# Kernel optimization log

Measured on AMD Instinct MI355X. Metric: run time of the kernel, lower is better.

## Reference

```python
import jax, jax.numpy as jnp
import numpy as np
import math

NUM_GRIDS = 128
INPUT_DIM = 128
OUTPUT_DIM = 128
BATCH = 8192
INIT_SCALE = 0.1


def _borders_cdf_grid(n_chunks):
    # inverse Laplace CDF grid borders, exactly as in the torch module
    def inv(u):
        return np.log(2.0 * u) if u <= 0.5 else -np.log(2.0 * (1.0 - u))
    cs = 1.0 / n_chunks
    b = [inv(i * cs) for i in range(1, n_chunks)]
    left = b[0] - (b[1] - b[0])
    right = b[-1] + (b[-1] - b[-2])
    return np.array([left] + b + [right], dtype=np.float32)  # [n_chunks+1]


def setup_inputs() -> dict:
    key = jax.random.key(0)
    kx, kp = jax.random.split(key)
    x = jax.random.normal(kx, (INPUT_DIM, BATCH), dtype=jnp.float32)
    s = INIT_SCALE / math.sqrt(INPUT_DIM)
    func_parameter = jax.random.uniform(
        kp, (NUM_GRIDS + 1, OUTPUT_DIM, INPUT_DIM), dtype=jnp.float32,
        minval=-s, maxval=s)
    borders = jnp.asarray(_borders_cdf_grid(NUM_GRIDS))
    inverse_chunk_lengths = 1.0 / (borders[1:] - borders[:-1])  # [NUM_GRIDS]
    return {"x": x, "func_parameter": func_parameter,
            "borders": borders, "inverse_chunk_lengths": inverse_chunk_lengths}


def reference(x, func_parameter, borders, inverse_chunk_lengths):
    # x: [I, B]; func_parameter: [G+1, O, I]
    G = borders.shape[0] - 1
    I = x.shape[0]
    # Laplace CDF: R -> [0, 1]
    exp_na = jnp.exp(-jnp.abs(x))
    cdf = jnp.where(x > 0, 1.0 - 0.5 * exp_na, 0.5 * exp_na)
    # bucketize on uniform CDF grid (truncation == floor since cdf*G >= 0)
    idx = jnp.clip((cdf * G).astype(jnp.int32), 0, G - 1)        # [I, B]
    idx_next = jnp.clip(idx + 1, 0, G)                           # [I, B]
    left = borders[idx]                                          # [I, B]
    inv_len = inverse_chunk_lengths[idx]                         # [I, B]
    d = (x - left) * inv_len                                     # [I, B]
    # gather per-input-dim parameter rows: val[i, b, o] = P[idx[i,b], o, i]
    Pt = jnp.transpose(func_parameter, (2, 0, 1))                # [I, G+1, O]
    rows = jnp.arange(I)[:, None]                                # [I, 1]
    val_l = Pt[rows, idx]                                        # [I, B, O]
    val_r = Pt[rows, idx_next]                                   # [I, B, O]
    out = ((1.0 - d)[..., None] * val_l + d[..., None] * val_r).sum(axis=0)  # [B, O]
    return out.T                                                 # [O, B]
```

## Files before the change

kernel.cpp:

```cpp
#include <hip/hip_runtime.h>
#include <cstdint>


#define NG 128
#define NI 128
#define NO 128
#define NB 8192

using half2v = __attribute__((ext_vector_type(2))) _Float16;

__device__ inline uint32_t pack_f16x2(float lo, float hi) {
    _Float16 hl = (_Float16)lo, hh = (_Float16)hi;
    return (uint32_t)__builtin_bit_cast(unsigned short, hl) |
           ((uint32_t)__builtin_bit_cast(unsigned short, hh) << 16);
}

__global__ __launch_bounds__(256) void build_q(const float* __restrict__ P,
                                               uint32_t* __restrict__ Q) {
    __shared__ float lp[32][129];
    __shared__ float ln[32][129];
    const int g  = blockIdx.x >> 2;
    const int o0 = (blockIdx.x & 3) * 32;
    const int t  = threadIdx.x;
    #pragma unroll
    for (int p = 0; p < 16; ++p) {
        int e = p * 256 + t;
        int ol = e >> 7, i = e & 127;
        lp[ol][i] = P[(size_t)(g * NO + o0 + ol) * NI + i];
        ln[ol][i] = P[(size_t)((g + 1) * NO + o0 + ol) * NI + i];
    }
    __syncthreads();
    #pragma unroll
    for (int p = 0; p < 16; ++p) {
        int e = p * 256 + t;
        int i = e >> 5, ol = e & 31;
        float pl = lp[ol][i];
        float dd = ln[ol][i] - pl;
        Q[((size_t)i * NG + g) * NO + o0 + ol] = pack_f16x2(pl, dd);
    }
}

__global__ __launch_bounds__(256) void build_t(const float* __restrict__ x,
                                               const float* __restrict__ borders,
                                               const float* __restrict__ icl,
                                               uint32_t* __restrict__ T) {
    __shared__ uint32_t lt[32][33];
    const int bi = blockIdx.x & 3;
    const int bb = blockIdx.x >> 2;
    const int t  = threadIdx.x;
    #pragma unroll
    for (int p = 0; p < 4; ++p) {
        int e = p * 256 + t;
        int il = e >> 5, bl = e & 31;
        float xv = x[(size_t)(bi * 32 + il) * NB + bb * 32 + bl];
        float ea = __expf(-fabsf(xv));
        float cdf = xv > 0.f ? 1.f - 0.5f * ea : 0.5f * ea;
        int idx = (int)(cdf * 128.f);
        idx = idx > 127 ? 127 : idx;
        float d = (xv - borders[idx]) * icl[idx];
        _Float16 hd = (_Float16)d;
        lt[il][bl] = (uint32_t)idx |
                     ((uint32_t)__builtin_bit_cast(unsigned short, hd) << 16);
    }
    __syncthreads();
    #pragma unroll
    for (int p = 0; p < 4; ++p) {
        int e = p * 256 + t;
        int bl = e >> 5, il = e & 31;
        T[(size_t)(bb * 32 + bl) * NI + bi * 32 + il] = lt[il][bl];
    }
}

__global__ __launch_bounds__(256) void main_k(const uint32_t* __restrict__ Q,
                                              const uint32_t* __restrict__ T,
                                              float* __restrict__ out) {
    __shared__ float sout[4][129];
    const int t    = threadIdx.x;
    const int wv   = t >> 6;
    const int lane = t & 63;
    const int b0   = blockIdx.x * 4;
    int b = __builtin_amdgcn_readfirstlane(b0 + wv);
    const uint32_t* __restrict__ trow = T + (size_t)b * NI;
    const int o0 = lane * 2;
    float acc0 = 0.f, acc1 = 0.f;
    #pragma unroll 8
    for (int i = 0; i < NI; ++i) {
        uint32_t tw  = trow[i];
        uint32_t idx = tw & 0xFFFFu;
        uint32_t wb  = (tw & 0xFFFF0000u) | 0x3C00u;
        const uint32_t* qrow = Q + ((size_t)((i << 7) + (int)idx) << 7);
        uint32_t q0 = qrow[o0];
        uint32_t q1 = qrow[o0 + 1];
        half2v w2 = __builtin_bit_cast(half2v, wb);
        acc0 = __builtin_amdgcn_fdot2(__builtin_bit_cast(half2v, q0), w2, acc0, false);
        acc1 = __builtin_amdgcn_fdot2(__builtin_bit_cast(half2v, q1), w2, acc1, false);
    }
    sout[wv][o0]     = acc0;
    sout[wv][o0 + 1] = acc1;
    __syncthreads();
    #pragma unroll
    for (int p = 0; p < 2; ++p) {
        int e = p * 256 + t;
        int bl = e & 3, o = e >> 2;
        out[(size_t)o * NB + b0 + bl] = sout[bl][o];
    }
}

extern "C" void kernel_launch(void* const* d_in, const int* in_sizes, int n_in,
                              void* d_out, int out_size, void* d_ws, size_t ws_size,
                              hipStream_t stream) {
    const float* x       = (const float*)d_in[0];
    const float* P       = (const float*)d_in[1];
    const float* borders = (const float*)d_in[2];
    const float* icl     = (const float*)d_in[3];
    float* out = (float*)d_out;

    uint32_t* Q = (uint32_t*)d_ws;
    uint32_t* T = Q + (size_t)NI * NG * NO;

    hipLaunchKernelGGL(build_q, dim3(NG * 4), dim3(256), 0, stream, P, Q);
    hipLaunchKernelGGL(build_t, dim3((NB / 32) * 4), dim3(256), 0, stream,
                       x, borders, icl, T);
    hipLaunchKernelGGL(main_k, dim3(NB / 4), dim3(256), 0, stream, Q, T, out);
}
```

Baseline: 111.7 us.

## Keep T in input-major layout and split main kernel over output slices

build_t now writes T in x's natural [I,B] layout with vectorized float4 loads and uint4 stores, dropping the shared-memory transpose. main_k is restructured so each block covers 32 batch columns and a 16-wide output slice: 8 lanes share one batch element and each lane loads a uint2 of Q. The output tile is then written coalesced along the batch dimension with nontemporal stores. This is meant to give better output coalescing and locality in the Q gather, at the cost of more gather instructions per useful output and a T read strided by NB.

```diff
diff --git a/kernel.cpp b/kernel.cpp
--- a/kernel.cpp
+++ b/kernel.cpp
@@ -44,65 +44,62 @@
                                                const float* __restrict__ borders,
                                                const float* __restrict__ icl,
                                                uint32_t* __restrict__ T) {
-    __shared__ uint32_t lt[32][33];
-    const int bi = blockIdx.x & 3;
-    const int bb = blockIdx.x >> 2;
-    const int t  = threadIdx.x;
+    const int e0 = (blockIdx.x * 256 + threadIdx.x) * 4;
+    const float4 xv = *(const float4*)(x + e0);
+    uint32_t r[4];
+    const float xs[4] = {xv.x, xv.y, xv.z, xv.w};
     #pragma unroll
-    for (int p = 0; p < 4; ++p) {
-        int e = p * 256 + t;
-        int il = e >> 5, bl = e & 31;
-        float xv = x[(size_t)(bi * 32 + il) * NB + bb * 32 + bl];
-        float ea = __expf(-fabsf(xv));
-        float cdf = xv > 0.f ? 1.f - 0.5f * ea : 0.5f * ea;
+    for (int k = 0; k < 4; ++k) {
+        float v = xs[k];
+        float ea = __expf(-fabsf(v));
+        float cdf = v > 0.f ? 1.f - 0.5f * ea : 0.5f * ea;
         int idx = (int)(cdf * 128.f);
         idx = idx > 127 ? 127 : idx;
-        float d = (xv - borders[idx]) * icl[idx];
+        float d = (v - borders[idx]) * icl[idx];
         _Float16 hd = (_Float16)d;
-        lt[il][bl] = (uint32_t)idx |
-                     ((uint32_t)__builtin_bit_cast(unsigned short, hd) << 16);
+        r[k] = (uint32_t)idx |
+               ((uint32_t)__builtin_bit_cast(unsigned short, hd) << 16);
     }
-    __syncthreads();
-    #pragma unroll
-    for (int p = 0; p < 4; ++p) {
-        int e = p * 256 + t;
-        int bl = e >> 5, il = e & 31;
-        T[(size_t)(bb * 32 + bl) * NI + bi * 32 + il] = lt[il][bl];
-    }
+    *(uint4*)(T + e0) = make_uint4(r[0], r[1], r[2], r[3]);
 }
 
 __global__ __launch_bounds__(256) void main_k(const uint32_t* __restrict__ Q,
                                               const uint32_t* __restrict__ T,
                                               float* __restrict__ out) {
-    __shared__ float sout[4][129];
-    const int t    = threadIdx.x;
-    const int wv   = t >> 6;
-    const int lane = t & 63;
-    const int b0   = blockIdx.x * 4;
-    int b = __builtin_amdgcn_readfirstlane(b0 + wv);
-    const uint32_t* __restrict__ trow = T + (size_t)b * NI;
-    const int o0 = lane * 2;
+    __shared__ float sout[32][17];
+    const int t     = threadIdx.x;
+    const int wv    = t >> 6;
+    const int lane  = t & 63;
+    const int slice = blockIdx.x & 7;
+    const int jb    = blockIdx.x >> 3;
+    const int bblk  = jb * 32;
+    const int o0    = slice * 16;
+    const int grp   = lane >> 3;
+    const int bme   = bblk + wv * 8 + grp;
+    const uint32_t lane_const = (uint32_t)(o0 * 4 + (lane & 7) * 8);
+
+    const char* Qb = (const char*)Q;
     float acc0 = 0.f, acc1 = 0.f;
     #pragma unroll 8
     for (int i = 0; i < NI; ++i) {
-        uint32_t tw  = trow[i];
+        uint32_t tw  = T[(size_t)i * NB + bme];
         uint32_t idx = tw & 0xFFFFu;
         uint32_t wb  = (tw & 0xFFFF0000u) | 0x3C00u;
-        const uint32_t* qrow = Q + ((size_t)((i << 7) + (int)idx) << 7);
-        uint32_t q0 = qrow[o0];
-        uint32_t q1 = qrow[o0 + 1];
+        uint2 q = *(const uint2*)(Qb + ((size_t)i << 16) + (idx << 9) + lane_const);
         half2v w2 = __builtin_bit_cast(half2v, wb);
-        acc0 = __builtin_amdgcn_fdot2(__builtin_bit_cast(half2v, q0), w2, acc0, false);
-        acc1 = __builtin_amdgcn_fdot2(__builtin_bit_cast(half2v, q1), w2, acc1, false);
+        acc0 = __builtin_amdgcn_fdot2(__builtin_bit_cast(half2v, q.x), w2, acc0, false);
+        acc1 = __builtin_amdgcn_fdot2(__builtin_bit_cast(half2v, q.y), w2, acc1, false);
     }
-    sout[wv][o0]     = acc0;
-    sout[wv][o0 + 1] = acc1;
+    const int oc = (lane & 7) * 2;
+    sout[wv * 8 + grp][oc]     = acc0;
+    sout[wv * 8 + grp][oc + 1] = acc1;
     __syncthreads();
     #pragma unroll
     for (int p = 0; p < 2; ++p) {
         int e = p * 256 + t;
-        int bl = e & 3, o = e >> 2;
-        out[(size_t)o * NB + b0 + bl] = sout[bl][o];
+        int ol = e >> 5, bl = e & 31;
+        __builtin_nontemporal_store(sout[bl][ol],
+                                    &out[(size_t)(o0 + ol) * NB + bblk + bl]);
     }
 }
 
@@ -119,7 +116,7 @@
     uint32_t* T = Q + (size_t)NI * NG * NO;
 
     hipLaunchKernelGGL(build_q, dim3(NG * 4), dim3(256), 0, stream, P, Q);
-    hipLaunchKernelGGL(build_t, dim3((NB / 32) * 4), dim3(256), 0, stream,
+    hipLaunchKernelGGL(build_t, dim3(NI * NB / 1024), dim3(256), 0, stream,
                        x, borders, icl, T);
     hipLaunchKernelGGL(main_k, dim3(NB / 4), dim3(256), 0, stream, Q, T, out);
 }
```

Measured after the change: 129.0 us. 15.5% more time.
